# Kernel optimization log

Hardware: AMD Instinct MI355X
Metric: run time of the kernel (lower is better)

Reference implementation:

```python
import jax, jax.numpy as jnp
import numpy as np

DIM = 1024
HEADS = 16
DIM_HEAD = 64


def setup_inputs() -> dict:
    key = jax.random.key(0)
    ks = jax.random.split(key, 6)
    inner = HEADS * DIM_HEAD  # 1024
    s = lambda fan_in: 1.0 / np.sqrt(fan_in)
    return {
        "x": jax.random.normal(ks[0], (4, 4096, DIM), dtype=jnp.float32),
        # weights stored as (in, out): y = x @ W (+ b), equivalent to torch Linear
        "W_qkv": jax.random.normal(ks[1], (DIM, inner * 3), dtype=jnp.float32) * s(DIM),
        "W_f": jax.random.normal(ks[2], (DIM_HEAD, DIM_HEAD), dtype=jnp.float32) * s(DIM_HEAD),
        "b_f": jax.random.normal(ks[3], (DIM_HEAD,), dtype=jnp.float32) * 0.01,
        "W_out": jax.random.normal(ks[4], (inner, DIM), dtype=jnp.float32) * s(inner),
        "b_out": jax.random.normal(ks[5], (DIM,), dtype=jnp.float32) * 0.01,
    }


def reference(x, W_qkv, W_f, b_f, W_out, b_out):
    B, N, C = x.shape
    H, D = HEADS, DIM_HEAD
    qkv = x @ W_qkv  # [B, N, 3*H*D]
    q, k, v = jnp.split(qkv, 3, axis=-1)
    # [B, N, H*D] -> [B, H, N, D]
    reshape = lambda t: t.reshape(B, N, H, D).transpose(0, 2, 1, 3)
    q, k, v = reshape(q), reshape(k), reshape(v)
    # shared feature map: Linear + ReLU applied per-head-dim
    fmap = lambda t: jax.nn.relu(t @ W_f + b_f)
    q = fmap(q)
    k = fmap(k)
    # KV summarization: O(N * D^2)
    kv = jnp.einsum('bhnd,bhne->bhde', k, v)       # [B, H, D, D]
    out = jnp.einsum('bhnd,bhde->bhne', q, kv)     # [B, H, N, D]
    # normalizer: q . sum_n k  (sum over sequence dim)
    k_sum = k.sum(axis=2)                          # [B, H, D]
    normalizer = jnp.einsum('bhnd,bhd->bhn', q, k_sum)
    out = out / (normalizer[..., None] + 1e-6)
    out = out.transpose(0, 2, 1, 3).reshape(B, N, H * D)
    return out @ W_out + b_out
```

## Files before the change

### kernel.cpp

```cpp
#include <hip/hip_runtime.h>
#include <hip/hip_bf16.h>
#include <stdint.h>

#define HEADS 16
#define DHEAD 64
#define DIM   1024
#define SEQ   4096
#define BATCH 4
#define MROWS (BATCH * SEQ)
#define NQKV  (3 * DIM)

typedef short  s16x8 __attribute__((ext_vector_type(8)));
typedef short  s16x4 __attribute__((ext_vector_type(4)));
typedef float  f32x4 __attribute__((ext_vector_type(4)));
typedef unsigned short u16;

__device__ __forceinline__ u16 f2bf(float f) {
  union { float f; uint32_t u; } v; v.f = f;
  uint32_t r = v.u + 0x7fffu + ((v.u >> 16) & 1u);
  return (u16)(r >> 16);
}
__device__ __forceinline__ float bf2f(u16 h) {
  union { uint32_t u; float f; } v; v.u = ((uint32_t)h) << 16;
  return v.f;
}

__device__ __forceinline__ void gload_lds16(const void* g, void* l) {
  __builtin_amdgcn_global_load_lds((__attribute__((address_space(1))) void*)(g),
                                   (__attribute__((address_space(3))) void*)(l),
                                   16, 0, 0);
}

__global__ __launch_bounds__(256) void cast_f32_bf16(const float* __restrict__ src,
                                                     u16* __restrict__ dst, int n) {
  int i = (blockIdx.x * 256 + threadIdx.x) * 4;
  const int stride = gridDim.x * 256 * 4;
  for (; i < n; i += stride) {
    float4 f = *(const float4*)(src + i);
    ushort4 o;
    o.x = f2bf(f.x); o.y = f2bf(f.y); o.z = f2bf(f.z); o.w = f2bf(f.w);
    *(ushort4*)(dst + i) = o;
  }
}

__global__ __launch_bounds__(256) void fold_qk(const float* __restrict__ Wqkv,
                                               const float* __restrict__ Wf,
                                               u16* __restrict__ WqkvT) {
  const int rh  = blockIdx.x >> 3;
  const int kc  = (blockIdx.x & 7) << 7;
  const int reg = rh >> 4, h = rh & 15;
  const int base = reg * DIM + h * DHEAD;
  __shared__ float wc[128 * 64];
  const int tid = threadIdx.x;
  const int j  = tid & 63;
  const int kg = tid >> 6;
  for (int i = tid; i < 128 * 16; i += 256) {
    const int r = i >> 4, c4 = (i & 15) << 2;
    *(float4*)&wc[r * 64 + c4] = *(const float4*)&Wqkv[(size_t)(kc + r) * NQKV + base + c4];
  }
  float v[64];
#pragma unroll
  for (int d = 0; d < 64; d++) v[d] = Wf[d * 64 + j];
  __syncthreads();
  u16* dst = WqkvT + (size_t)(base + j) * DIM + kc + kg * 32;
  for (int ki = 0; ki < 32; ki++) {
    const int k = kg * 32 + ki;
    float s = 0.f;
#pragma unroll
    for (int d = 0; d < 64; d++) s += wc[k * 64 + d] * v[d];
    dst[ki] = f2bf(s);
  }
}

__global__ __launch_bounds__(256) void transpose_cast(const float* __restrict__ src,
                                                      int srcStride, int colOff,
                                                      u16* __restrict__ dst, int Nt) {
  __shared__ float t[64][65];
  const int ntiles = Nt >> 6;
  const int n0 = (blockIdx.x % ntiles) * 64;
  const int k0 = (blockIdx.x / ntiles) * 64;
  for (int i = threadIdx.x; i < 4096; i += 256) {
    const int r = i >> 6, c = i & 63;
    t[r][c] = src[(size_t)(k0 + r) * srcStride + colOff + n0 + c];
  }
  __syncthreads();
  for (int i = threadIdx.x; i < 4096; i += 256) {
    const int r = i & 63, c = i >> 6;
    dst[(size_t)(n0 + c) * DIM + k0 + r] = f2bf(t[r][c]);
  }
}

template <int EPI>
__global__ __launch_bounds__(512, 2) void gemm8p(const u16* __restrict__ A,
                                                 const u16* __restrict__ Bt,
                                                 void* __restrict__ Cout,
                                                 const float* __restrict__ bias,
                                                 int Nn, int K) {
  __shared__ __align__(16) u16 smem[2][2][2][128 * 64];
  const int tilesN = Nn >> 8;
  const int cpx   = gridDim.x >> 3;
  const int xcd   = blockIdx.x & 7;
  const int local = blockIdx.x >> 3;
  const int bmPerX = cpx / tilesN;
  const int perG = 4 * tilesN;
  const int g = local / perG, rrm = local % perG;
  const int bm = xcd * bmPerX + g * 4 + rrm / tilesN;
  const int bn = rrm % tilesN;
  const int m0 = bm << 8, n0 = bn << 8;

  const int tid  = threadIdx.x;
  const int lane = tid & 63;
  const int w    = tid >> 6;
  const int wr = w >> 2, wcn = w & 3;
  const int lrow = lane & 15;
  const int hi   = lane >> 4;
  const int sx   = lrow & 7;

  const int srow  = tid >> 3;
  const int pslot = tid & 7;
  const int gk    = (pslot ^ (srow & 7)) << 3;
  const u16* aBase = A  + (size_t)m0 * K + gk;
  const u16* bBase = Bt + (size_t)n0 * K + gk;

#define STG(buf, op, half, kt, gb)                                             \
  { const u16* s0_ = (gb) + (size_t)((half) * 128 + srow) * K + (kt) * 64;     \
    char* d0_ = (char*)&smem[buf][op][half][0] + tid * 16;                     \
    gload_lds16(s0_, d0_);                                                     \
    gload_lds16(s0_ + (size_t)64 * K, d0_ + 8192); }

#define RDA(buf, dst, mbase)                                                   \
  _Pragma("unroll") for (int mi_ = 0; mi_ < 4; mi_++)                          \
  _Pragma("unroll") for (int kk_ = 0; kk_ < 2; kk_++) {                        \
    const int r_ = ((mbase) + mi_) * 16 + lrow;                                \
    dst[mi_][kk_] = *(const s16x8*)&smem[buf][0][wr]                           \
                        [r_ * 64 + ((kk_ * 4 + hi) ^ sx) * 8]; }

#define RDB(buf, dst, nbase)                                                   \
  _Pragma("unroll") for (int nj_ = 0; nj_ < 2; nj_++)                          \
  _Pragma("unroll") for (int kk_ = 0; kk_ < 2; kk_++) {                        \
    const int r_ = (wcn & 1) * 64 + ((nbase) + nj_) * 16 + lrow;               \
    dst[nj_][kk_] = *(const s16x8*)&smem[buf][1][wcn >> 1]                     \
                        [r_ * 64 + ((kk_ * 4 + hi) ^ sx) * 8]; }

#define MM(mbase, nbase, areg, breg)                                           \
  _Pragma("unroll") for (int mi_ = 0; mi_ < 4; mi_++)                          \
  _Pragma("unroll") for (int nj_ = 0; nj_ < 2; nj_++)                          \
  _Pragma("unroll") for (int kk_ = 0; kk_ < 2; kk_++)                          \
    acc[(mbase) + mi_][(nbase) + nj_] = __builtin_amdgcn_mfma_f32_16x16x32_bf16( \
        breg[nj_][kk_], areg[mi_][kk_], acc[(mbase) + mi_][(nbase) + nj_], 0, 0, 0);

#define WLG  asm volatile("s_waitcnt lgkmcnt(0)" ::: "memory")
#define WVM8 asm volatile("s_waitcnt vmcnt(8)" ::: "memory")
#define WVM0 asm volatile("s_waitcnt vmcnt(0)" ::: "memory")
#define BAR  __builtin_amdgcn_s_barrier()
#define PRIO1 __builtin_amdgcn_s_setprio(1)
#define PRIO0 __builtin_amdgcn_s_setprio(0)

  f32x4 acc[8][4] = {};
  const int NT  = K >> 6;
  const int NIT = NT >> 1;

  STG(0, 0, 0, 0, aBase); STG(0, 0, 1, 0, aBase);
  STG(0, 1, 0, 0, bBase); STG(0, 1, 1, 0, bBase);
  STG(1, 0, 0, 1, aBase); STG(1, 0, 1, 1, aBase);
  STG(1, 1, 0, 1, bBase); STG(1, 1, 1, 1, bBase);
  WVM8; BAR;

  for (int it = 0; it < NIT; ++it) {
    const int tE = 2 * it + 2, tO = 2 * it + 3;
    const bool pf = (tE < NT);
    s16x8 a[4][2], bl[2][2], bh[2][2];
    RDA(0, a, 0); RDB(0, bl, 0);
    BAR; WLG;
    PRIO1; MM(0, 0, a, bl); PRIO0;
    BAR;
    RDB(0, bh, 2);
    BAR; WLG;
    PRIO1; MM(0, 2, a, bh); PRIO0;
    BAR;
    RDA(0, a, 4);
    if (pf) { STG(0, 1, 0, tE, bBase); STG(0, 1, 1, tE, bBase); }
    BAR; WLG;
    PRIO1; MM(4, 2, a, bh); PRIO0;
    BAR;
    if (pf) { STG(0, 0, 0, tE, aBase); STG(0, 0, 1, tE, aBase); }
    BAR;
    if (pf) { WVM8; } else { WVM0; }
    PRIO1; MM(4, 0, a, bl); PRIO0;
    BAR;
    RDA(1, a, 0); RDB(1, bl, 0);
    BAR; WLG;
    PRIO1; MM(0, 0, a, bl); PRIO0;
    BAR;
    RDB(1, bh, 2);
    BAR; WLG;
    PRIO1; MM(0, 2, a, bh); PRIO0;
    BAR;
    RDA(1, a, 4);
    if (pf) { STG(1, 1, 0, tO, bBase); STG(1, 1, 1, tO, bBase); }
    BAR; WLG;
    PRIO1; MM(4, 2, a, bh); PRIO0;
    BAR;
    if (pf) { STG(1, 0, 0, tO, aBase); STG(1, 0, 1, tO, aBase); }
    BAR;
    if (pf) { WVM8; } else { WVM0; }
    PRIO1; MM(4, 0, a, bl); PRIO0;
    BAR;
  }

  const int mrow = m0 + wr * 128 + lrow;
  const int nb0  = n0 + wcn * 64 + (hi << 2);
#pragma unroll
  for (int mi = 0; mi < 8; mi++) {
    const int row = mrow + mi * 16;
#pragma unroll
    for (int nj = 0; nj < 4; nj++) {
      const int nb = nb0 + nj * 16;
      float v0 = acc[mi][nj][0], v1 = acc[mi][nj][1];
      float v2 = acc[mi][nj][2], v3 = acc[mi][nj][3];
      if (EPI == 1) {
        if (nb < 2 * DIM) {
          const int bb = nb & 63;
          v0 += bias[bb];     v1 += bias[bb + 1];
          v2 += bias[bb + 2]; v3 += bias[bb + 3];
          v0 = v0 > 0.f ? v0 : 0.f;  v1 = v1 > 0.f ? v1 : 0.f;
          v2 = v2 > 0.f ? v2 : 0.f;  v3 = v3 > 0.f ? v3 : 0.f;
        }
        uint2 st;
        st.x = (uint32_t)f2bf(v0) | ((uint32_t)f2bf(v1) << 16);
        st.y = (uint32_t)f2bf(v2) | ((uint32_t)f2bf(v3) << 16);
        *(uint2*)((u16*)Cout + (size_t)row * Nn + nb) = st;
      } else {
        float4 st;
        st.x = v0 + bias[nb];     st.y = v1 + bias[nb + 1];
        st.z = v2 + bias[nb + 2]; st.w = v3 + bias[nb + 3];
        *(float4*)((float*)Cout + (size_t)row * Nn + nb) = st;
      }
    }
  }
#undef STG
#undef RDA
#undef RDB
#undef MM
#undef WLG
#undef WVM8
#undef WVM0
#undef BAR
#undef PRIO1
#undef PRIO0
}

__global__ __launch_bounds__(256) void kv_ksum_mfma(const u16* __restrict__ qkv,
                                                    float* __restrict__ kvpart,
                                                    float* __restrict__ kspart) {
  const int bh = blockIdx.x >> 3;
  const int chunk = blockIdx.x & 7;
  const int b = bh >> 4, h = bh & 15;
  __shared__ u16 kT[64 * 64];
  __shared__ u16 vT[80 * 64];
  const int tid  = threadIdx.x;
  const int lane = tid & 63;
  const int w    = tid >> 6;
  const int lrow = lane & 15;
  const int hi   = lane >> 4;

  for (int i = tid; i < 16 * 64; i += 256) {
    const int r = 64 + (i >> 6), n = i & 63;
    vT[r * 64 + (((n >> 3) ^ (r & 7)) << 3) + (n & 7)] = (r == 64) ? (u16)0x3F80 : (u16)0;
  }

  f32x4 acc[5] = {};
  const u16* kbase = qkv + (size_t)(b * SEQ) * NQKV + DIM     + h * DHEAD;
  const u16* vbase = qkv + (size_t)(b * SEQ) * NQKV + 2 * DIM + h * DHEAD;

  for (int r0 = chunk * 512; r0 < chunk * 512 + 512; r0 += 64) {
    __syncthreads();
    for (int s = tid; s < 512; s += 256) {
      const int r  = s >> 3;
      const int c0 = (s & 7) << 3;
      const s16x8 k8 = *(const s16x8*)(kbase + (size_t)(r0 + r) * NQKV + c0);
      const s16x8 v8 = *(const s16x8*)(vbase + (size_t)(r0 + r) * NQKV + c0);
      const int slot = r >> 3, nb = r & 7;
#pragma unroll
      for (int q = 0; q < 8; q++) {
        const int d = c0 + q;
        const int off = d * 64 + ((slot ^ (d & 7)) << 3) + nb;
        kT[off] = (u16)k8[q];
        vT[off] = (u16)v8[q];
      }
    }
    __syncthreads();
#pragma unroll
    for (int kk = 0; kk < 2; kk++) {
      const int drow = w * 16 + lrow;
      const s16x8 kf = *(const s16x8*)&kT[drow * 64 + (((kk * 4 + hi) ^ (drow & 7)) << 3)];
#pragma unroll
      for (int et = 0; et < 5; et++) {
        const int erow = et * 16 + lrow;
        const s16x8 vf = *(const s16x8*)&vT[erow * 64 + (((kk * 4 + hi) ^ (erow & 7)) << 3)];
        acc[et] = __builtin_amdgcn_mfma_f32_16x16x32_bf16(vf, kf, acc[et], 0, 0, 0);
      }
    }
  }

  const int d = w * 16 + lrow;
  float* outp = kvpart + (size_t)blockIdx.x * 4096;
#pragma unroll
  for (int et = 0; et < 4; et++)
    *(f32x4*)&outp[d * 64 + et * 16 + hi * 4] = acc[et];
  if (hi == 0) kspart[(size_t)blockIdx.x * 64 + d] = acc[4][0];
}

__global__ __launch_bounds__(256) void reduce_kv(const float* __restrict__ kvpart,
                                                 const float* __restrict__ kspart,
                                                 float* __restrict__ kvbuf,
                                                 float* __restrict__ ksumb) {
  const int idx = blockIdx.x * 256 + threadIdx.x;
  if (idx < 64 * 4096) {
    const int bh = idx >> 12, i = idx & 4095;
    float s = 0.f;
#pragma unroll
    for (int c = 0; c < 8; c++) s += kvpart[(size_t)((bh << 3) + c) * 4096 + i];
    kvbuf[idx] = s;
  } else {
    const int idx2 = idx - 64 * 4096;
    if (idx2 < 4096) {
      const int bh = idx2 >> 6, i = idx2 & 63;
      float s = 0.f;
#pragma unroll
      for (int c = 0; c < 8; c++) s += kspart[((bh << 3) + c) * 64 + i];
      ksumb[idx2] = s;
    }
  }
}

__global__ __launch_bounds__(256) void attn_mfma(const u16* __restrict__ qkv,
                                                 const float* __restrict__ kvbuf,
                                                 const float* __restrict__ ksumb,
                                                 u16* __restrict__ attn) {
  const int bh = blockIdx.x >> 4;
  const int mc = blockIdx.x & 15;
  const int b = bh >> 4, h = bh & 15;
  __shared__ u16 BT[2][80][64];
  __shared__ float nrm[256];
  const int tid  = threadIdx.x;
  const int lane = tid & 63;
  const int w    = tid >> 6;
  const int lrow = lane & 15;
  const int hi   = lane >> 4;

#pragma unroll
  for (int s = 0; s < 20; s++) {
    const int idx = tid + 256 * s;
    const int e = idx >> 6, d = idx & 63;
    float v;
    if (e < 64)       v = kvbuf[(size_t)bh * 4096 + d * 64 + e];
    else if (e == 64) v = ksumb[bh * 64 + d];
    else              v = 0.f;
    const u16 vh = f2bf(v);
    const u16 vl = f2bf(v - bf2f(vh));
    const int off = e * 64 + (((d >> 3) ^ (e & 7)) << 3) + (d & 7);
    BT[0][0][off] = vh;
    BT[1][0][off] = vl;
  }

  const int rloc = w * 64 + lrow;
  const u16* qbase = qkv + (size_t)(b * SEQ + mc * 256 + rloc) * NQKV + h * DHEAD + hi * 8;
  s16x8 af[4][2];
#pragma unroll
  for (int mi = 0; mi < 4; mi++)
#pragma unroll
    for (int kk = 0; kk < 2; kk++)
      af[mi][kk] = *(const s16x8*)(qbase + (size_t)(mi * 16) * NQKV + kk * 32);

  __syncthreads();

  f32x4 acc[4][5] = {};
#pragma unroll
  for (int wv = 0; wv < 2; wv++) {
#pragma unroll
    for (int jb = 0; jb < 5; jb++) {
      const int erow = jb * 16 + lrow;
      const int sx = erow & 7;
      s16x8 bq0 = *(const s16x8*)&BT[wv][erow][((0 * 4 + hi) ^ sx) << 3];
      s16x8 bq1 = *(const s16x8*)&BT[wv][erow][((1 * 4 + hi) ^ sx) << 3];
#pragma unroll
      for (int mi = 0; mi < 4; mi++) {
        acc[mi][jb] = __builtin_amdgcn_mfma_f32_16x16x32_bf16(bq0, af[mi][0], acc[mi][jb], 0, 0, 0);
        acc[mi][jb] = __builtin_amdgcn_mfma_f32_16x16x32_bf16(bq1, af[mi][1], acc[mi][jb], 0, 0, 0);
      }
    }
  }

  if (hi == 0) {
#pragma unroll
    for (int mi = 0; mi < 4; mi++) nrm[rloc + mi * 16] = acc[mi][4][0] + 1e-6f;
  }
  __syncthreads();

  u16* obase = attn + (size_t)(b * SEQ + mc * 256 + rloc) * DIM + h * DHEAD + hi * 4;
#pragma unroll
  for (int mi = 0; mi < 4; mi++) {
    const float sc = 1.f / nrm[rloc + mi * 16];
#pragma unroll
    for (int jb = 0; jb < 4; jb++) {
      uint2 st;
      st.x = (uint32_t)f2bf(acc[mi][jb][0] * sc) | ((uint32_t)f2bf(acc[mi][jb][1] * sc) << 16);
      st.y = (uint32_t)f2bf(acc[mi][jb][2] * sc) | ((uint32_t)f2bf(acc[mi][jb][3] * sc) << 16);
      *(uint2*)(obase + (size_t)(mi * 16) * DIM + jb * 16) = st;
    }
  }
}

extern "C" void kernel_launch(void* const* d_in, const int* in_sizes, int n_in,
                              void* d_out, int out_size, void* d_ws, size_t ws_size,
                              hipStream_t stream) {
  (void)in_sizes; (void)n_in; (void)out_size; (void)ws_size;
  const float* x     = (const float*)d_in[0];
  const float* Wqkv  = (const float*)d_in[1];
  const float* Wf    = (const float*)d_in[2];
  const float* bfv   = (const float*)d_in[3];
  const float* Wout  = (const float*)d_in[4];
  const float* bout  = (const float*)d_in[5];
  float* out = (float*)d_out;
  char* ws = (char*)d_ws;

  u16*   wqkvT = (u16*)(ws + 0);
  u16*   woutT = (u16*)(ws + 6291456);
  u16*   xb    = (u16*)(ws + 8388608);
  u16*   qkvb  = (u16*)(ws + 41943040);
  u16*   attn  = (u16*)(ws + 142606336);
  float* kvp   = (float*)(ws + 176160768);
  float* ksp   = (float*)(ws + 184549376);
  float* kvbuf = (float*)(ws + 184680448);
  float* ksumb = (float*)(ws + 185729024);

  cast_f32_bf16<<<2048, 256, 0, stream>>>(x, xb, MROWS * DIM);
  fold_qk<<<256, 256, 0, stream>>>(Wqkv, Wf, wqkvT);
  transpose_cast<<<256, 256, 0, stream>>>(Wqkv, NQKV, 2 * DIM, wqkvT + (size_t)2 * DIM * DIM, DIM);
  transpose_cast<<<256, 256, 0, stream>>>(Wout, DIM, 0, woutT, DIM);
  gemm8p<1><<<(MROWS / 256) * (NQKV / 256), 512, 0, stream>>>(xb, wqkvT, qkvb, bfv,
                                                              NQKV, DIM);
  kv_ksum_mfma<<<64 * 8, 256, 0, stream>>>(qkvb, kvp, ksp);
  reduce_kv<<<(64 * 4096 + 64 * 64 + 255) / 256, 256, 0, stream>>>(kvp, ksp, kvbuf, ksumb);
  attn_mfma<<<64 * 16, 256, 0, stream>>>(qkvb, kvbuf, ksumb, attn);
  gemm8p<2><<<(MROWS / 256) * (DIM / 256), 512, 0, stream>>>(attn, woutT, out, bout,
                                                             DIM, DIM);
}
```

Baseline: 256.1 us.

## Restructure GEMM main loop into four phases with deferred A-tile prefetch

The bf16 MFMA GEMM main loop is cut from eight barrier-separated compute phases per iteration to four. Each phase now issues the LDS reads for both B halves together and runs two MFMA groups back to back. The odd-buffer A-tile global prefetch moves to the start of the next iteration, and the vmcnt wait is tightened from 8 to 4. The aim is fewer barriers and LDS waits and more overlap between global loads and MFMA work. The cost is more live registers, and the reordered prefetch and vmcnt accounting could cause stalls or hazards if the counts are off.

```diff
diff --git a/kernel.cpp b/kernel.cpp
--- a/kernel.cpp
+++ b/kernel.cpp
@@ -91,7 +91,7 @@
 }
 
 template <int EPI>
-__global__ __launch_bounds__(512, 2) void gemm8p(const u16* __restrict__ A,
+__global__ __launch_bounds__(512, 2) void gemm4p(const u16* __restrict__ A,
                                                  const u16* __restrict__ Bt,
                                                  void* __restrict__ Cout,
                                                  const float* __restrict__ bias,
@@ -151,6 +151,7 @@
 
 #define WLG  asm volatile("s_waitcnt lgkmcnt(0)" ::: "memory")
 #define WVM8 asm volatile("s_waitcnt vmcnt(8)" ::: "memory")
+#define WVM4 asm volatile("s_waitcnt vmcnt(4)" ::: "memory")
 #define WVM0 asm volatile("s_waitcnt vmcnt(0)" ::: "memory")
 #define BAR  __builtin_amdgcn_s_barrier()
 #define PRIO1 __builtin_amdgcn_s_setprio(1)
@@ -170,41 +171,29 @@
     const int tE = 2 * it + 2, tO = 2 * it + 3;
     const bool pf = (tE < NT);
     s16x8 a[4][2], bl[2][2], bh[2][2];
-    RDA(0, a, 0); RDB(0, bl, 0);
+    RDA(0, a, 0); RDB(0, bl, 0); RDB(0, bh, 2);
+    if (it > 0) { STG(1, 0, 0, 2 * it + 1, aBase); STG(1, 0, 1, 2 * it + 1, aBase); }
     BAR; WLG;
-    PRIO1; MM(0, 0, a, bl); PRIO0;
-    BAR;
-    RDB(0, bh, 2);
-    BAR; WLG;
-    PRIO1; MM(0, 2, a, bh); PRIO0;
+    PRIO1; MM(0, 0, a, bl); MM(0, 2, a, bh); PRIO0;
     BAR;
     RDA(0, a, 4);
     if (pf) { STG(0, 1, 0, tE, bBase); STG(0, 1, 1, tE, bBase); }
+    BAR;
+    if (pf) { WVM4; } else { WVM0; }
+    WLG;
+    PRIO1; MM(4, 0, a, bl); MM(4, 2, a, bh); PRIO0;
+    BAR;
+    RDA(1, a, 0); RDB(1, bl, 0); RDB(1, bh, 2);
+    if (pf) { STG(0, 0, 0, tE, aBase); STG(0, 0, 1, tE, aBase); }
     BAR; WLG;
-    PRIO1; MM(4, 2, a, bh); PRIO0;
-    BAR;
-    if (pf) { STG(0, 0, 0, tE, aBase); STG(0, 0, 1, tE, aBase); }
-    BAR;
-    if (pf) { WVM8; } else { WVM0; }
-    PRIO1; MM(4, 0, a, bl); PRIO0;
-    BAR;
-    RDA(1, a, 0); RDB(1, bl, 0);
-    BAR; WLG;
-    PRIO1; MM(0, 0, a, bl); PRIO0;
-    BAR;
-    RDB(1, bh, 2);
-    BAR; WLG;
-    PRIO1; MM(0, 2, a, bh); PRIO0;
+    PRIO1; MM(0, 0, a, bl); MM(0, 2, a, bh); PRIO0;
     BAR;
     RDA(1, a, 4);
     if (pf) { STG(1, 1, 0, tO, bBase); STG(1, 1, 1, tO, bBase); }
-    BAR; WLG;
-    PRIO1; MM(4, 2, a, bh); PRIO0;
-    BAR;
-    if (pf) { STG(1, 0, 0, tO, aBase); STG(1, 0, 1, tO, aBase); }
-    BAR;
-    if (pf) { WVM8; } else { WVM0; }
-    PRIO1; MM(4, 0, a, bl); PRIO0;
+    BAR;
+    if (pf) { WVM4; } else { WVM0; }
+    WLG;
+    PRIO1; MM(4, 0, a, bl); MM(4, 2, a, bh); PRIO0;
     BAR;
   }
 
@@ -244,6 +233,7 @@
 #undef MM
 #undef WLG
 #undef WVM8
+#undef WVM4
 #undef WVM0
 #undef BAR
 #undef PRIO1
@@ -439,11 +429,11 @@
   fold_qk<<<256, 256, 0, stream>>>(Wqkv, Wf, wqkvT);
   transpose_cast<<<256, 256, 0, stream>>>(Wqkv, NQKV, 2 * DIM, wqkvT + (size_t)2 * DIM * DIM, DIM);
   transpose_cast<<<256, 256, 0, stream>>>(Wout, DIM, 0, woutT, DIM);
-  gemm8p<1><<<(MROWS / 256) * (NQKV / 256), 512, 0, stream>>>(xb, wqkvT, qkvb, bfv,
+  gemm4p<1><<<(MROWS / 256) * (NQKV / 256), 512, 0, stream>>>(xb, wqkvT, qkvb, bfv,
                                                               NQKV, DIM);
   kv_ksum_mfma<<<64 * 8, 256, 0, stream>>>(qkvb, kvp, ksp);
   reduce_kv<<<(64 * 4096 + 64 * 64 + 255) / 256, 256, 0, stream>>>(kvp, ksp, kvbuf, ksumb);
   attn_mfma<<<64 * 16, 256, 0, stream>>>(qkvb, kvbuf, ksumb, attn);
-  gemm8p<2><<<(MROWS / 256) * (DIM / 256), 512, 0, stream>>>(attn, woutT, out, bout,
+  gemm4p<2><<<(MROWS / 256) * (DIM / 256), 512, 0, stream>>>(attn, woutT, out, bout,
                                                              DIM, DIM);
 }
```

Result: no change. 257.0 us (+0.3%).
